# Performance work log

Hardware: AMD Instinct MI355X
Metric: run time of the kernel (lower is better)

Reference implementation:

```python
import jax, jax.numpy as jnp
import numpy as np


def setup_inputs() -> dict:
    key = jax.random.key(0)
    ks = jax.random.split(key, 4)
    B, C, D, H, W = 2, 128, 16, 16, 16
    scale = 1.0 / np.sqrt(C)
    x = jax.random.normal(ks[0], (B, C, D, H, W), dtype=jnp.float32)
    Wq = jax.random.normal(ks[1], (C, C), dtype=jnp.float32) * scale
    Wk = jax.random.normal(ks[2], (C, C), dtype=jnp.float32) * scale
    Wv = jax.random.normal(ks[3], (C, C), dtype=jnp.float32) * scale
    bq = jnp.zeros((C,), jnp.float32)
    bk = jnp.zeros((C,), jnp.float32)
    bv = jnp.zeros((C,), jnp.float32)
    gamma = jnp.asarray(0.3, jnp.float32)
    return {"x": x, "Wq": Wq, "bq": bq, "Wk": Wk, "bk": bk, "Wv": Wv, "bv": bv, "gamma": gamma}


def reference(x, Wq, bq, Wk, bk, Wv, bv, gamma):
    B, C, D, H, W = x.shape
    N = D * H * W
    xf = x.reshape(B, C, N)  # flatten spatial dims
    # 1x1x1 Conv3d == per-voxel channel mixing
    q = jnp.einsum('oc,bcn->bon', Wq, xf) + bq[:, None]
    k = jnp.einsum('oc,bcn->bon', Wk, xf) + bk[:, None]
    v = jnp.einsum('oc,bcn->bon', Wv, xf) + bv[:, None]
    # attn[b,n,m] = sum_c q[b,c,n] * k[b,c,m], custom 1.3 scale, softmax over m
    attn = jax.nn.softmax(jnp.einsum('bcn,bcm->bnm', q, k) * 1.3, axis=2)
    # out = v @ attn^T : out[b,c,n] = sum_m v[b,c,m] * attn[b,n,m]
    out = jnp.einsum('bcm,bnm->bcn', v, attn)
    return x + gamma * out.reshape(B, C, D, H, W)
```

## Files before the change

### kernel.cpp

```cpp
#include <hip/hip_runtime.h>
#include <hip/hip_bf16.h>

typedef __bf16 bf16x8 __attribute__((ext_vector_type(8)));
typedef __bf16 bf16x4 __attribute__((ext_vector_type(4)));
typedef float  floatx4 __attribute__((ext_vector_type(4)));


#define QSCALE 1.8755035f

__global__ __launch_bounds__(128) void proj_kernel(
    const float* __restrict__ x,
    const float* __restrict__ Wq, const float* __restrict__ bq,
    const float* __restrict__ Wk, const float* __restrict__ bk,
    const float* __restrict__ Wv, const float* __restrict__ bv,
    __bf16* __restrict__ qT, __bf16* __restrict__ kT, __bf16* __restrict__ vT2)
{
    constexpr int C = 128, N = 4096;
    const int b = blockIdx.z, which = blockIdx.y, n0 = blockIdx.x * 32;
    const int tid = threadIdx.x;
    const int wv = tid >> 6, lane = tid & 63, l15 = lane & 15, quad = lane >> 4;
    const float* W    = (which == 0) ? Wq : (which == 1) ? Wk : Wv;
    const float* bias = (which == 0) ? bq : (which == 1) ? bk : bv;

    __shared__ __bf16 xhi[32][136];
    __shared__ __bf16 xlo[32][136];
    __shared__ __bf16 v_lds[128][40];

    #pragma unroll
    for (int rep = 0; rep < 8; ++rep) {
        const int j = tid + rep * 128;
        const int c = j >> 3, nl4 = (j & 7) * 4;
        const float4 xv = *(const float4*)(x + (size_t)(b * C + c) * N + n0 + nl4);
        #pragma unroll
        for (int r = 0; r < 4; ++r) {
            const float v = (&xv.x)[r];
            const __bf16 h = (__bf16)v;
            xhi[nl4 + r][c] = h;
            xlo[nl4 + r][c] = (__bf16)(v - (float)h);
        }
    }
    __syncthreads();

    bf16x8 xbh[4], xbl[4];
    #pragma unroll
    for (int kk = 0; kk < 4; ++kk) {
        xbh[kk] = *(bf16x8*)(&xhi[wv * 16 + l15][kk * 32 + quad * 8]);
        xbl[kk] = *(bf16x8*)(&xlo[wv * 16 + l15][kk * 32 + quad * 8]);
    }

    floatx4 acc[8];
    const floatx4 fz = {0.f, 0.f, 0.f, 0.f};
    #pragma unroll
    for (int t = 0; t < 8; ++t) acc[t] = fz;

    #pragma unroll
    for (int kk = 0; kk < 4; ++kk)
        #pragma unroll
        for (int ct = 0; ct < 8; ++ct) {
            const float* wp = W + (size_t)(ct * 16 + l15) * C + kk * 32 + quad * 8;
            const float4 w0 = *(const float4*)wp;
            const float4 w1 = *(const float4*)(wp + 4);
            bf16x8 ahi, alo;
            #pragma unroll
            for (int r = 0; r < 4; ++r) {
                const float v0 = (&w0.x)[r]; const __bf16 h0 = (__bf16)v0;
                ahi[r] = h0; alo[r] = (__bf16)(v0 - (float)h0);
                const float v1 = (&w1.x)[r]; const __bf16 h1 = (__bf16)v1;
                ahi[4 + r] = h1; alo[4 + r] = (__bf16)(v1 - (float)h1);
            }
            acc[ct] = __builtin_amdgcn_mfma_f32_16x16x32_bf16(ahi, xbh[kk], acc[ct], 0, 0, 0);
            acc[ct] = __builtin_amdgcn_mfma_f32_16x16x32_bf16(alo, xbh[kk], acc[ct], 0, 0, 0);
            acc[ct] = __builtin_amdgcn_mfma_f32_16x16x32_bf16(ahi, xbl[kk], acc[ct], 0, 0, 0);
        }

    const int n = n0 + wv * 16 + l15;
    if (which < 2) {
        __bf16* dst = (which == 0) ? qT : kT;
        #pragma unroll
        for (int ct = 0; ct < 8; ++ct) {
            const float4 b4 = *(const float4*)(bias + ct * 16 + quad * 4);
            bf16x4 o;
            #pragma unroll
            for (int r = 0; r < 4; ++r) o[r] = (__bf16)(acc[ct][r] + (&b4.x)[r]);
            *(bf16x4*)(dst + (size_t)(b * N + n) * C + ct * 16 + quad * 4) = o;
        }
    } else {
        #pragma unroll
        for (int ct = 0; ct < 8; ++ct) {
            const float4 b4 = *(const float4*)(bias + ct * 16 + quad * 4);
            #pragma unroll
            for (int r = 0; r < 4; ++r)
                v_lds[ct * 16 + quad * 4 + r][wv * 16 + l15] = (__bf16)(acc[ct][r] + (&b4.x)[r]);
        }
        __syncthreads();
        #pragma unroll
        for (int rep = 0; rep < 4; ++rep) {
            const int j = tid + rep * 128;
            const int c = j >> 2, m8 = (j & 3) * 8;
            *(bf16x8*)(vT2 + (size_t)(b * C + c) * N + n0 + m8) = *(bf16x8*)(&v_lds[c][m8]);
        }
    }
}

template <int NSPLIT, bool PARTIAL>
__global__ __launch_bounds__(256, 2) void flash_kernel(
    const __bf16* __restrict__ qT, const __bf16* __restrict__ kT,
    const __bf16* __restrict__ vT2, const float* __restrict__ x,
    const float* __restrict__ gamma_p, __bf16* __restrict__ Opart,
    float* __restrict__ ml, float* __restrict__ out)
{
    constexpr int C = 128, N = 4096, Bn = 2;
    const int bid = blockIdx.x;
    const int r7 = bid & 7;
    const int b = r7 >> 2;
    const int rest = (bid >> 3) * 4 + (r7 & 3);
    const int nt = rest / NSPLIT, split = rest % NSPLIT;
    const int n0 = nt * 128;
    const int tid = threadIdx.x;
    const int wv = tid >> 6, lane = tid & 63, l15 = lane & 15, quad = lane >> 4;

    __shared__ __bf16 k_s[64][136];
    __shared__ __bf16 v_s[128][72];
    __shared__ __bf16 p_s[4][32][72];

    const int nA = n0 + wv * 32 + l15;
    bf16x8 qbA[4], qbB[4];
    #pragma unroll
    for (int kk = 0; kk < 4; ++kk) {
        qbA[kk] = *(const bf16x8*)(qT + (size_t)(b * N + nA) * C + kk * 32 + quad * 8);
        qbB[kk] = *(const bf16x8*)(qT + (size_t)(b * N + nA + 16) * C + kk * 32 + quad * 8);
    }

    float mA = -3.0e38f, lA = 0.f, mB = -3.0e38f, lB = 0.f;
    floatx4 OA[8], OB[8];
    const floatx4 fz = {0.f, 0.f, 0.f, 0.f};
    #pragma unroll
    for (int t = 0; t < 8; ++t) { OA[t] = fz; OB[t] = fz; }

    const __bf16* kB = kT  + (size_t)b * N * C;
    const __bf16* vB = vT2 + (size_t)b * C * N;
    constexpr int ITERS = (N / NSPLIT) / 64;
    const int mbeg = split * (N / NSPLIT);

    bf16x8 kpre[4], vpre[4];
    #pragma unroll
    for (int rep = 0; rep < 4; ++rep) {
        const int kj = tid + rep * 256;
        kpre[rep] = *(const bf16x8*)(kB + (size_t)(mbeg + (kj >> 4)) * C + (kj & 15) * 8);
        const int vj = tid + rep * 256;
        vpre[rep] = *(const bf16x8*)(vB + (size_t)(vj >> 3) * N + mbeg + (vj & 7) * 8);
    }

    for (int it = 0; it < ITERS; ++it) {
        __syncthreads();
        #pragma unroll
        for (int rep = 0; rep < 4; ++rep) {
            const int kj = tid + rep * 256;
            *(bf16x8*)(&k_s[kj >> 4][(kj & 15) * 8]) = kpre[rep];
            const int vj = tid + rep * 256;
            *(bf16x8*)(&v_s[vj >> 3][(vj & 7) * 8]) = vpre[rep];
        }
        __syncthreads();

        if (it + 1 < ITERS) {
            const int m1 = mbeg + (it + 1) * 64;
            #pragma unroll
            for (int rep = 0; rep < 4; ++rep) {
                const int kj = tid + rep * 256;
                kpre[rep] = *(const bf16x8*)(kB + (size_t)(m1 + (kj >> 4)) * C + (kj & 15) * 8);
                const int vj = tid + rep * 256;
                vpre[rep] = *(const bf16x8*)(vB + (size_t)(vj >> 3) * N + m1 + (vj & 7) * 8);
            }
        }

        floatx4 SA[4], SB[4];
        #pragma unroll
        for (int ct = 0; ct < 4; ++ct) { SA[ct] = fz; SB[ct] = fz; }
        #pragma unroll
        for (int kk = 0; kk < 4; ++kk)
            #pragma unroll
            for (int ct = 0; ct < 4; ++ct) {
                const bf16x8 a = *(bf16x8*)(&k_s[ct * 16 + l15][kk * 32 + quad * 8]);
                SA[ct] = __builtin_amdgcn_mfma_f32_16x16x32_bf16(a, qbA[kk], SA[ct], 0, 0, 0);
                SB[ct] = __builtin_amdgcn_mfma_f32_16x16x32_bf16(a, qbB[kk], SB[ct], 0, 0, 0);
            }

        float rmaxA = -3.0e38f, rmaxB = -3.0e38f;
        #pragma unroll
        for (int ct = 0; ct < 4; ++ct)
            #pragma unroll
            for (int r = 0; r < 4; ++r) {
                rmaxA = fmaxf(rmaxA, SA[ct][r]);
                rmaxB = fmaxf(rmaxB, SB[ct][r]);
            }
        rmaxA = fmaxf(rmaxA, __shfl_xor(rmaxA, 16, 64));
        rmaxA = fmaxf(rmaxA, __shfl_xor(rmaxA, 32, 64));
        rmaxB = fmaxf(rmaxB, __shfl_xor(rmaxB, 16, 64));
        rmaxB = fmaxf(rmaxB, __shfl_xor(rmaxB, 32, 64));

        const float mnA = fmaxf(mA, rmaxA);
        const float alphaA = exp2f((mA - mnA) * QSCALE);
        mA = mnA;
        const float mnB = fmaxf(mB, rmaxB);
        const float alphaB = exp2f((mB - mnB) * QSCALE);
        mB = mnB;
        const float qmA = mA * QSCALE, qmB = mB * QSCALE;

        float rsumA = 0.f, rsumB = 0.f;
        #pragma unroll
        for (int ct = 0; ct < 4; ++ct)
            #pragma unroll
            for (int r = 0; r < 4; ++r) {
                const float pA = exp2f(SA[ct][r] * QSCALE - qmA); SA[ct][r] = pA; rsumA += pA;
                const float pB = exp2f(SB[ct][r] * QSCALE - qmB); SB[ct][r] = pB; rsumB += pB;
            }
        rsumA += __shfl_xor(rsumA, 16, 64);
        rsumA += __shfl_xor(rsumA, 32, 64);
        rsumB += __shfl_xor(rsumB, 16, 64);
        rsumB += __shfl_xor(rsumB, 32, 64);
        lA = lA * alphaA + rsumA;
        lB = lB * alphaB + rsumB;

        #pragma unroll
        for (int t = 0; t < 8; ++t)
            #pragma unroll
            for (int r = 0; r < 4; ++r) { OA[t][r] *= alphaA; OB[t][r] *= alphaB; }

        #pragma unroll
        for (int ct = 0; ct < 4; ++ct) {
            bf16x4 pkA, pkB;
            #pragma unroll
            for (int r = 0; r < 4; ++r) { pkA[r] = (__bf16)SA[ct][r]; pkB[r] = (__bf16)SB[ct][r]; }
            *(bf16x4*)(&p_s[wv][l15][ct * 16 + quad * 4])      = pkA;
            *(bf16x4*)(&p_s[wv][16 + l15][ct * 16 + quad * 4]) = pkB;
        }

        #pragma unroll
        for (int kk = 0; kk < 2; ++kk) {
            const bf16x8 pbA = *(bf16x8*)(&p_s[wv][l15][kk * 32 + quad * 8]);
            const bf16x8 pbB = *(bf16x8*)(&p_s[wv][16 + l15][kk * 32 + quad * 8]);
            #pragma unroll
            for (int ct = 0; ct < 8; ++ct) {
                const bf16x8 a = *(bf16x8*)(&v_s[ct * 16 + l15][kk * 32 + quad * 8]);
                OA[ct] = __builtin_amdgcn_mfma_f32_16x16x32_bf16(a, pbA, OA[ct], 0, 0, 0);
                OB[ct] = __builtin_amdgcn_mfma_f32_16x16x32_bf16(a, pbB, OB[ct], 0, 0, 0);
            }
        }
    }

    if (PARTIAL) {
        __bf16* OpA = Opart + (((size_t)split * Bn + b) * N + nA) * C;
        __bf16* OpB = OpA + (size_t)16 * C;
        #pragma unroll
        for (int ct = 0; ct < 8; ++ct) {
            bf16x4 oA, oB;
            #pragma unroll
            for (int r = 0; r < 4; ++r) { oA[r] = (__bf16)OA[ct][r]; oB[r] = (__bf16)OB[ct][r]; }
            *(bf16x4*)(OpA + ct * 16 + quad * 4) = oA;
            *(bf16x4*)(OpB + ct * 16 + quad * 4) = oB;
        }
        if (quad == 0) {
            float* mlp = ml + (((size_t)split * Bn + b) * N + nA) * 2;
            mlp[0] = mA; mlp[1] = lA;
            mlp[32] = mB; mlp[33] = lB;
        }
    } else {
        const float scA = 1.f / lA, scB = 1.f / lB;
        const float gamma = gamma_p[0];
        #pragma unroll
        for (int ct = 0; ct < 8; ++ct)
            #pragma unroll
            for (int r = 0; r < 4; ++r) {
                const int c = ct * 16 + quad * 4 + r;
                const size_t iA = ((size_t)b * C + c) * N + nA;
                out[iA]      = x[iA]      + gamma * OA[ct][r] * scA;
                out[iA + 16] = x[iA + 16] + gamma * OB[ct][r] * scB;
            }
    }
}

template <int S>
__global__ __launch_bounds__(128) void combine_kernel(
    const __bf16* __restrict__ Opart, const float* __restrict__ ml,
    const float* __restrict__ x, const float* __restrict__ gamma_p,
    float* __restrict__ out)
{
    constexpr int C = 128, N = 4096, Bn = 2;
    const int b = blockIdx.y, n0 = blockIdx.x * 16;
    const int tid = threadIdx.x;
    __shared__ float cf[S][16];
    __shared__ float ot[16][132];

    if (tid < 16) {
        const int n = n0 + tid;
        float ms[S], ls[S];
        #pragma unroll
        for (int s = 0; s < S; ++s) {
            const float* mlp = ml + (((size_t)s * Bn + b) * N + n) * 2;
            ms[s] = mlp[0]; ls[s] = mlp[1];
        }
        float M = -3.0e38f;
        #pragma unroll
        for (int s = 0; s < S; ++s) M = fmaxf(M, ms[s]);
        float L = 0.f, e[S];
        #pragma unroll
        for (int s = 0; s < S; ++s) { e[s] = exp2f((ms[s] - M) * QSCALE); L += e[s] * ls[s]; }
        const float inv = 1.f / L;
        #pragma unroll
        for (int s = 0; s < S; ++s) cf[s][tid] = e[s] * inv;
    }
    __syncthreads();

    #pragma unroll
    for (int rep = 0; rep < 2; ++rep) {
        const int j = tid + rep * 128;
        const int nl = j >> 4, c8 = (j & 15) * 8;
        float acc[8] = {0, 0, 0, 0, 0, 0, 0, 0};
        #pragma unroll
        for (int s = 0; s < S; ++s) {
            const float c0 = cf[s][nl];
            const bf16x8 ov = *(const bf16x8*)(Opart + (((size_t)s * Bn + b) * N + n0 + nl) * C + c8);
            #pragma unroll
            for (int t = 0; t < 8; ++t) acc[t] += c0 * (float)ov[t];
        }
        *(float4*)(&ot[nl][c8])     = *(float4*)(&acc[0]);
        *(float4*)(&ot[nl][c8 + 4]) = *(float4*)(&acc[4]);
    }
    __syncthreads();

    const int nl = tid & 15, cbase = tid >> 4;
    const float gamma = gamma_p[0];
    #pragma unroll
    for (int k = 0; k < 16; ++k) {
        const int c = cbase * 16 + k;
        const size_t idx = ((size_t)b * C + c) * N + n0 + nl;
        out[idx] = x[idx] + gamma * ot[nl][c];
    }
}

extern "C" void kernel_launch(void* const* d_in, const int* in_sizes, int n_in,
                              void* d_out, int out_size, void* d_ws, size_t ws_size,
                              hipStream_t stream) {
    const float* x     = (const float*)d_in[0];
    const float* Wq    = (const float*)d_in[1];
    const float* bq    = (const float*)d_in[2];
    const float* Wk    = (const float*)d_in[3];
    const float* bk    = (const float*)d_in[4];
    const float* Wv    = (const float*)d_in[5];
    const float* bv    = (const float*)d_in[6];
    const float* gamma = (const float*)d_in[7];
    float* out = (float*)d_out;

    constexpr int Bn = 2, C = 128, N = 4096;
    constexpr size_t QKV = (size_t)Bn * N * C;
    __bf16* qT    = (__bf16*)d_ws;
    __bf16* kT    = qT + QKV;
    __bf16* vT2   = kT + QKV;
    __bf16* Opart = vT2 + QKV;
    float* ml8 = (float*)(Opart + (size_t)8 * Bn * N * C);
    float* ml4 = (float*)(Opart + (size_t)4 * Bn * N * C);
    const size_t need8 = (char*)(ml8 + (size_t)8 * Bn * N * 2) - (char*)d_ws;
    const size_t need4 = (char*)(ml4 + (size_t)4 * Bn * N * 2) - (char*)d_ws;

    proj_kernel<<<dim3(N / 32, 3, Bn), 128, 0, stream>>>(
        x, Wq, bq, Wk, bk, Wv, bv, qT, kT, vT2);

    if (ws_size >= need8) {
        flash_kernel<8, true><<<32 * 8 * Bn, 256, 0, stream>>>(
            qT, kT, vT2, x, gamma, Opart, ml8, out);
        combine_kernel<8><<<dim3(N / 16, Bn), 128, 0, stream>>>(
            Opart, ml8, x, gamma, out);
    } else if (ws_size >= need4) {
        flash_kernel<4, true><<<32 * 4 * Bn, 256, 0, stream>>>(
            qT, kT, vT2, x, gamma, Opart, ml4, out);
        combine_kernel<4><<<dim3(N / 16, Bn), 128, 0, stream>>>(
            Opart, ml4, x, gamma, out);
    } else {
        flash_kernel<1, false><<<32 * 1 * Bn, 256, 0, stream>>>(
            qT, kT, vT2, x, gamma, nullptr, nullptr, out);
    }
}
```

Measured before the change: 122.5 us.

## Pre-split weights to bf16 hi/lo once and double projection tile per block

Adds a prep kernel that converts the three weight matrices into bf16 hi/lo halves once in the workspace, so the projection kernel loads ready bf16 vectors instead of re-splitting fp32 weights in every block. The projection tile grows from 32 to 64 voxels per block, and each wave computes two 16-column sub-tiles that share the same weight fragments, halving weight reloads. This costs an extra kernel launch, more LDS and registers per block, and half as many blocks (fewer waves in flight).

```diff
diff --git a/kernel.cpp b/kernel.cpp
--- a/kernel.cpp
+++ b/kernel.cpp
@@ -8,28 +8,41 @@
 
 #define QSCALE 1.8755035f
 
+__global__ __launch_bounds__(256) void prep_w(
+    const float* __restrict__ Wq, const float* __restrict__ Wk,
+    const float* __restrict__ Wv, __bf16* __restrict__ Whi, __bf16* __restrict__ Wlo)
+{
+    const int idx = blockIdx.x * 256 + threadIdx.x;
+    const int which = idx >> 14, rem = idx & 16383;
+    const float w = (which == 0 ? Wq : which == 1 ? Wk : Wv)[rem];
+    const __bf16 hi = (__bf16)w;
+    Whi[idx] = hi;
+    Wlo[idx] = (__bf16)(w - (float)hi);
+}
+
 __global__ __launch_bounds__(128) void proj_kernel(
     const float* __restrict__ x,
-    const float* __restrict__ Wq, const float* __restrict__ bq,
-    const float* __restrict__ Wk, const float* __restrict__ bk,
-    const float* __restrict__ Wv, const float* __restrict__ bv,
+    const __bf16* __restrict__ Whi, const __bf16* __restrict__ Wlo,
+    const float* __restrict__ bq, const float* __restrict__ bk,
+    const float* __restrict__ bv,
     __bf16* __restrict__ qT, __bf16* __restrict__ kT, __bf16* __restrict__ vT2)
 {
     constexpr int C = 128, N = 4096;
-    const int b = blockIdx.z, which = blockIdx.y, n0 = blockIdx.x * 32;
+    const int b = blockIdx.z, which = blockIdx.y, n0 = blockIdx.x * 64;
     const int tid = threadIdx.x;
     const int wv = tid >> 6, lane = tid & 63, l15 = lane & 15, quad = lane >> 4;
-    const float* W    = (which == 0) ? Wq : (which == 1) ? Wk : Wv;
     const float* bias = (which == 0) ? bq : (which == 1) ? bk : bv;
-
-    __shared__ __bf16 xhi[32][136];
-    __shared__ __bf16 xlo[32][136];
-    __shared__ __bf16 v_lds[128][40];
-
-    #pragma unroll
-    for (int rep = 0; rep < 8; ++rep) {
+    const __bf16* Wh = Whi + (size_t)which * 16384;
+    const __bf16* Wl = Wlo + (size_t)which * 16384;
+
+    __shared__ __bf16 xhi[64][136];
+    __shared__ __bf16 xlo[64][136];
+    __shared__ __bf16 v_lds[128][72];
+
+    #pragma unroll
+    for (int rep = 0; rep < 16; ++rep) {
         const int j = tid + rep * 128;
-        const int c = j >> 3, nl4 = (j & 7) * 4;
+        const int c = j >> 4, nl4 = (j & 15) * 4;
         const float4 xv = *(const float4*)(x + (size_t)(b * C + c) * N + n0 + nl4);
         #pragma unroll
         for (int r = 0; r < 4; ++r) {
@@ -41,62 +54,66 @@
     }
     __syncthreads();
 
-    bf16x8 xbh[4], xbl[4];
+    const int nlA = wv * 32 + l15;
+    bf16x8 xhA[4], xlA[4], xhB[4], xlB[4];
     #pragma unroll
     for (int kk = 0; kk < 4; ++kk) {
-        xbh[kk] = *(bf16x8*)(&xhi[wv * 16 + l15][kk * 32 + quad * 8]);
-        xbl[kk] = *(bf16x8*)(&xlo[wv * 16 + l15][kk * 32 + quad * 8]);
-    }
-
-    floatx4 acc[8];
+        xhA[kk] = *(bf16x8*)(&xhi[nlA][kk * 32 + quad * 8]);
+        xlA[kk] = *(bf16x8*)(&xlo[nlA][kk * 32 + quad * 8]);
+        xhB[kk] = *(bf16x8*)(&xhi[nlA + 16][kk * 32 + quad * 8]);
+        xlB[kk] = *(bf16x8*)(&xlo[nlA + 16][kk * 32 + quad * 8]);
+    }
+
+    floatx4 accA[8], accB[8];
     const floatx4 fz = {0.f, 0.f, 0.f, 0.f};
     #pragma unroll
-    for (int t = 0; t < 8; ++t) acc[t] = fz;
+    for (int t = 0; t < 8; ++t) { accA[t] = fz; accB[t] = fz; }
 
     #pragma unroll
     for (int kk = 0; kk < 4; ++kk)
         #pragma unroll
         for (int ct = 0; ct < 8; ++ct) {
-            const float* wp = W + (size_t)(ct * 16 + l15) * C + kk * 32 + quad * 8;
-            const float4 w0 = *(const float4*)wp;
-            const float4 w1 = *(const float4*)(wp + 4);
-            bf16x8 ahi, alo;
-            #pragma unroll
-            for (int r = 0; r < 4; ++r) {
-                const float v0 = (&w0.x)[r]; const __bf16 h0 = (__bf16)v0;
-                ahi[r] = h0; alo[r] = (__bf16)(v0 - (float)h0);
-                const float v1 = (&w1.x)[r]; const __bf16 h1 = (__bf16)v1;
-                ahi[4 + r] = h1; alo[4 + r] = (__bf16)(v1 - (float)h1);
-            }
-            acc[ct] = __builtin_amdgcn_mfma_f32_16x16x32_bf16(ahi, xbh[kk], acc[ct], 0, 0, 0);
-            acc[ct] = __builtin_amdgcn_mfma_f32_16x16x32_bf16(alo, xbh[kk], acc[ct], 0, 0, 0);
-            acc[ct] = __builtin_amdgcn_mfma_f32_16x16x32_bf16(ahi, xbl[kk], acc[ct], 0, 0, 0);
-        }
-
-    const int n = n0 + wv * 16 + l15;
+            const size_t wo = (size_t)(ct * 16 + l15) * C + kk * 32 + quad * 8;
+            const bf16x8 ahi = *(const bf16x8*)(Wh + wo);
+            const bf16x8 alo = *(const bf16x8*)(Wl + wo);
+            accA[ct] = __builtin_amdgcn_mfma_f32_16x16x32_bf16(ahi, xhA[kk], accA[ct], 0, 0, 0);
+            accA[ct] = __builtin_amdgcn_mfma_f32_16x16x32_bf16(alo, xhA[kk], accA[ct], 0, 0, 0);
+            accA[ct] = __builtin_amdgcn_mfma_f32_16x16x32_bf16(ahi, xlA[kk], accA[ct], 0, 0, 0);
+            accB[ct] = __builtin_amdgcn_mfma_f32_16x16x32_bf16(ahi, xhB[kk], accB[ct], 0, 0, 0);
+            accB[ct] = __builtin_amdgcn_mfma_f32_16x16x32_bf16(alo, xhB[kk], accB[ct], 0, 0, 0);
+            accB[ct] = __builtin_amdgcn_mfma_f32_16x16x32_bf16(ahi, xlB[kk], accB[ct], 0, 0, 0);
+        }
+
+    const int nA = n0 + nlA;
     if (which < 2) {
         __bf16* dst = (which == 0) ? qT : kT;
         #pragma unroll
         for (int ct = 0; ct < 8; ++ct) {
             const float4 b4 = *(const float4*)(bias + ct * 16 + quad * 4);
-            bf16x4 o;
-            #pragma unroll
-            for (int r = 0; r < 4; ++r) o[r] = (__bf16)(acc[ct][r] + (&b4.x)[r]);
-            *(bf16x4*)(dst + (size_t)(b * N + n) * C + ct * 16 + quad * 4) = o;
+            bf16x4 oA, oB;
+            #pragma unroll
+            for (int r = 0; r < 4; ++r) {
+                oA[r] = (__bf16)(accA[ct][r] + (&b4.x)[r]);
+                oB[r] = (__bf16)(accB[ct][r] + (&b4.x)[r]);
+            }
+            *(bf16x4*)(dst + (size_t)(b * N + nA) * C + ct * 16 + quad * 4) = oA;
+            *(bf16x4*)(dst + (size_t)(b * N + nA + 16) * C + ct * 16 + quad * 4) = oB;
         }
     } else {
         #pragma unroll
         for (int ct = 0; ct < 8; ++ct) {
             const float4 b4 = *(const float4*)(bias + ct * 16 + quad * 4);
             #pragma unroll
-            for (int r = 0; r < 4; ++r)
-                v_lds[ct * 16 + quad * 4 + r][wv * 16 + l15] = (__bf16)(acc[ct][r] + (&b4.x)[r]);
+            for (int r = 0; r < 4; ++r) {
+                v_lds[ct * 16 + quad * 4 + r][nlA]      = (__bf16)(accA[ct][r] + (&b4.x)[r]);
+                v_lds[ct * 16 + quad * 4 + r][nlA + 16] = (__bf16)(accB[ct][r] + (&b4.x)[r]);
+            }
         }
         __syncthreads();
         #pragma unroll
-        for (int rep = 0; rep < 4; ++rep) {
+        for (int rep = 0; rep < 8; ++rep) {
             const int j = tid + rep * 128;
-            const int c = j >> 2, m8 = (j & 3) * 8;
+            const int c = j >> 3, m8 = (j & 7) * 8;
             *(bf16x8*)(vT2 + (size_t)(b * C + c) * N + n0 + m8) = *(bf16x8*)(&v_lds[c][m8]);
         }
     }
@@ -356,14 +373,17 @@
     __bf16* qT    = (__bf16*)d_ws;
     __bf16* kT    = qT + QKV;
     __bf16* vT2   = kT + QKV;
-    __bf16* Opart = vT2 + QKV;
+    __bf16* Whi   = vT2 + QKV;
+    __bf16* Wlo   = Whi + 3 * 16384;
+    __bf16* Opart = Wlo + 3 * 16384;
     float* ml8 = (float*)(Opart + (size_t)8 * Bn * N * C);
     float* ml4 = (float*)(Opart + (size_t)4 * Bn * N * C);
     const size_t need8 = (char*)(ml8 + (size_t)8 * Bn * N * 2) - (char*)d_ws;
     const size_t need4 = (char*)(ml4 + (size_t)4 * Bn * N * 2) - (char*)d_ws;
 
-    proj_kernel<<<dim3(N / 32, 3, Bn), 128, 0, stream>>>(
-        x, Wq, bq, Wk, bk, Wv, bv, qT, kT, vT2);
+    prep_w<<<192, 256, 0, stream>>>(Wq, Wk, Wv, Whi, Wlo);
+    proj_kernel<<<dim3(N / 64, 3, Bn), 128, 0, stream>>>(
+        x, Whi, Wlo, bq, bk, bv, qT, kT, vT2);
 
     if (ws_size >= need8) {
         flash_kernel<8, true><<<32 * 8 * Bn, 256, 0, stream>>>(
```

Result: no change. 123.5 us (+0.8%).
